# Kernel optimization log

Measured on AMD Instinct MI355X. Metric: run time of the kernel, lower is better.

## Reference

```python
import jax, jax.numpy as jnp
import numpy as np
from jax import lax

STRIDES = (4, 8, 16, 32, 64)
SIZES = (32, 64, 128, 256, 512)
RATIOS = (0.5, 1.0, 2.0)
IMG_H, IMG_W = 1024, 1024
PRE_NMS = 1000
POST_NMS = 1000
NMS_THRESH = 0.7
BBOX_CLIP = float(np.log(1000.0 / 16.0))
NEG_INF = -1e9


def _cell_anchors(size):
    a = []
    for r in RATIOS:
        w = size * np.sqrt(1.0 / r)
        h = size * np.sqrt(r)
        a.append([-w / 2.0, -h / 2.0, w / 2.0, h / 2.0])
    return np.array(a, np.float32)  # [A,4]


def _level_anchors(H, W, stride, size):
    cell = _cell_anchors(size)  # [A,4]
    ys = np.arange(H, dtype=np.float32) * stride
    xs = np.arange(W, dtype=np.float32) * stride
    yy, xx = np.meshgrid(ys, xs, indexing='ij')  # row-major (H,W)
    shifts = np.stack([xx, yy, xx, yy], axis=-1).reshape(-1, 1, 4)
    return jnp.asarray((shifts + cell[None]).reshape(-1, 4))  # [(H*W*A),4] in (H,W,A) order


def conv2d(x, w, b, pad):
    y = lax.conv_general_dilated(x, w, (1, 1), pad,
                                 dimension_numbers=('NCHW', 'OIHW', 'NCHW'))
    return y + b[None, :, None, None]


def decode(deltas, anchors):
    widths = anchors[:, 2] - anchors[:, 0] + 1.0
    heights = anchors[:, 3] - anchors[:, 1] + 1.0
    ctr_x = anchors[:, 0] + 0.5 * widths
    ctr_y = anchors[:, 1] + 0.5 * heights
    dx, dy = deltas[..., 0], deltas[..., 1]
    dw = jnp.minimum(deltas[..., 2], BBOX_CLIP)
    dh = jnp.minimum(deltas[..., 3], BBOX_CLIP)
    pcx = dx * widths + ctr_x
    pcy = dy * heights + ctr_y
    pw = jnp.exp(dw) * widths
    ph = jnp.exp(dh) * heights
    return jnp.stack([pcx - 0.5 * pw, pcy - 0.5 * ph,
                      pcx + 0.5 * pw - 1.0, pcy + 0.5 * ph - 1.0], axis=-1)


def iou_matrix(boxes):
    area = (boxes[:, 2] - boxes[:, 0]) * (boxes[:, 3] - boxes[:, 1])
    lt = jnp.maximum(boxes[:, None, :2], boxes[None, :, :2])
    rb = jnp.minimum(boxes[:, None, 2:], boxes[None, :, 2:])
    wh = jnp.maximum(rb - lt, 0.0)
    inter = wh[..., 0] * wh[..., 1]
    return inter / (area[:, None] + area[None, :] - inter + 1e-9)


def nms_keep(boxes):
    # boxes [N,4] already sorted by score desc; greedy NMS -> bool keep mask
    N = boxes.shape[0]
    iou = iou_matrix(boxes)

    def body(keep, i):
        row = jnp.take(iou, i, axis=0) > NMS_THRESH
        row = row.at[i].set(False)
        keep = jnp.where(keep[i], keep & ~row, keep)
        return keep, None

    keep, _ = lax.scan(body, jnp.ones((N,), bool), jnp.arange(N))
    return keep


def _forward(feats, conv_w, conv_b, cls_w, cls_b, bbox_w, bbox_b):
    level_boxes, level_scores = [], []
    for lvl, feat in enumerate(feats):
        B, _, H, W = feat.shape
        t = jax.nn.relu(conv2d(feat, conv_w, conv_b, 'SAME'))
        logits = conv2d(t, cls_w, cls_b, 'VALID')    # [B,A,H,W]
        breg = conv2d(t, bbox_w, bbox_b, 'VALID')    # [B,4A,H,W]
        A = logits.shape[1]
        scores = jnp.transpose(logits, (0, 2, 3, 1)).reshape(B, -1)            # (H,W,A)
        deltas = breg.reshape(B, A, 4, H, W).transpose(0, 3, 4, 1, 2).reshape(B, -1, 4)
        anchors = _level_anchors(H, W, STRIDES[lvl], SIZES[lvl])
        boxes = decode(deltas, anchors)  # [B,N,4]
        boxes = jnp.stack([jnp.clip(boxes[..., 0], 0.0, IMG_W - 1.0),
                           jnp.clip(boxes[..., 1], 0.0, IMG_H - 1.0),
                           jnp.clip(boxes[..., 2], 0.0, IMG_W - 1.0),
                           jnp.clip(boxes[..., 3], 0.0, IMG_H - 1.0)], axis=-1)
        k = min(PRE_NMS, scores.shape[1])
        top_s, idx = lax.top_k(scores, k)                                   # [B,k]
        top_b = jnp.take_along_axis(boxes, idx[..., None], axis=1)          # [B,k,4]
        keep = jax.vmap(nms_keep)(top_b)                                    # [B,k] bool
        level_scores.append(jnp.where(keep, top_s, NEG_INF))
        level_boxes.append(top_b)
    all_s = jnp.concatenate(level_scores, axis=1)
    all_b = jnp.concatenate(level_boxes, axis=1)
    fs, fi = lax.top_k(all_s, POST_NMS)                                     # [B,POST]
    fb = jnp.take_along_axis(all_b, fi[..., None], axis=1)                  # [B,POST,4]
    return jnp.concatenate([fb, fs[..., None]], axis=-1)                    # [B,POST,5]


def setup_inputs() -> dict:
    key = jax.random.key(0)
    ks = jax.random.split(key, 8)
    C = 256
    feats = {
        'feat0': jax.random.normal(ks[0], (2, C, 256, 256), jnp.float32),
        'feat1': jax.random.normal(ks[1], (2, C, 128, 128), jnp.float32),
        'feat2': jax.random.normal(ks[2], (2, C, 64, 64), jnp.float32),
        'feat3': jax.random.normal(ks[3], (2, C, 32, 32), jnp.float32),
        'feat4': jax.random.normal(ks[4], (2, C, 16, 16), jnp.float32),
    }
    params = {
        'conv_w': jax.random.normal(ks[5], (C, C, 3, 3), jnp.float32) * 0.01,
        'conv_b': jnp.zeros((C,), jnp.float32),
        'cls_w': jax.random.normal(ks[6], (3, C, 1, 1), jnp.float32) * 0.01,
        'cls_b': jnp.zeros((3,), jnp.float32),
        'bbox_w': jax.random.normal(ks[7], (12, C, 1, 1), jnp.float32) * 0.01,
        'bbox_b': jnp.zeros((12,), jnp.float32),
    }
    return {**feats, **params}


def reference(feat0, feat1, feat2, feat3, feat4, conv_w, conv_b, cls_w, cls_b, bbox_w, bbox_b):
    return _forward([feat0, feat1, feat2, feat3, feat4],
                    conv_w, conv_b, cls_w, cls_b, bbox_w, bbox_b)
```

## Files before the change

### kernel.cpp

```cpp
#include <hip/hip_runtime.h>
#include <cmath>


#define NTOT_PER_IMG 261888
#define ATOT_PER_IMG 4768

__constant__ int c_NLVL[5] = {196608, 49152, 12288, 3072, 768};
__constant__ int c_KLVL[5] = {1000, 1000, 1000, 1000, 768};
__constant__ int c_LOFF[5] = {0, 196608, 245760, 258048, 261120};
__constant__ int c_AOFF[5] = {0, 1000, 2000, 3000, 4000};

struct Anch { float cx1[3]; float cy1[3]; };
struct ConvCfg { Anch an[5]; };

__device__ __forceinline__ void ldsWaveFence() {
  asm volatile("s_waitcnt lgkmcnt(0)" ::: "memory");
}

__global__ __launch_bounds__(256) void wtrans(const float* __restrict__ Wsrc,
                                              float* __restrict__ Wt) {
  __shared__ float T[16][17];
  int k0 = blockIdx.x * 16;
  int o0 = blockIdx.y * 16;
  int i = threadIdx.x >> 4, j = threadIdx.x & 15;
  T[i][j] = Wsrc[(size_t)(o0 + i) * 2304 + (k0 + j)];
  __syncthreads();
  Wt[(size_t)(k0 + i) * 256 + (o0 + j)] = T[j][i];
}

__global__ __launch_bounds__(256, 2) void conv_gemm(
    const float* __restrict__ f0, const float* __restrict__ f1,
    const float* __restrict__ f2, const float* __restrict__ f3,
    const float* __restrict__ f4, const float* __restrict__ Wt,
    const float* __restrict__ convb, const float* __restrict__ clsw,
    const float* __restrict__ clsb, const float* __restrict__ bboxw,
    const float* __restrict__ bboxb, float* __restrict__ scoresOut,
    float4* __restrict__ boxesOut, ConvCfg cfg) {
  __shared__ __align__(16) float s_mem[7424];
  __shared__ float s_Red2[272];
  float* const s_tl = s_mem;
  float* const s_xbase = s_mem + 4160;

  int b = blockIdx.x;
  const float* feat;
  int lvl, img, tile, H, logW, stride, lvlOff;
  if (b < 2048) {
    lvl = 0; feat = f0; H = 256; logW = 8; stride = 4; lvlOff = 0;
    img = b >> 10; tile = b & 1023;
  } else if (b < 2560) {
    lvl = 1; feat = f1; H = 128; logW = 7; stride = 8; lvlOff = 196608;
    int r = b - 2048; img = r >> 8; tile = r & 255;
  } else if (b < 2688) {
    lvl = 2; feat = f2; H = 64; logW = 6; stride = 16; lvlOff = 245760;
    int r = b - 2560; img = r >> 6; tile = r & 63;
  } else if (b < 2720) {
    lvl = 3; feat = f3; H = 32; logW = 5; stride = 32; lvlOff = 258048;
    int r = b - 2688; img = r >> 4; tile = r & 15;
  } else {
    lvl = 4; feat = f4; H = 16; logW = 4; stride = 64; lvlOff = 261120;
    int r = b - 2720; img = r >> 2; tile = r & 3;
  }
  const int W = H, HW = H * W;
  const int p0 = tile * 64;
  const float* fimg = feat + (size_t)img * 256 * HW;

  const int log2nc = (logW < 6) ? logW : 6;
  const int ncols = 1 << log2nc;
  const int R = 64 >> log2nc;
  const int py0 = p0 >> logW;
  const int c_start = p0 & (W - 1);
  const int WIN = ncols + 2;
  const int NX = (R + 2) * WIN;

  const int tid = threadIdx.x;
  const int wid = tid >> 6;
  const int lane = tid & 63;
  const int oc0 = (tid >> 3) * 8;
  const int pxg = tid & 7;
  const int px0 = pxg * 8;
  const int trow = px0 >> log2nc;
  const int tcol0 = px0 & (ncols - 1);

  float* const s_xw = s_xbase + wid * 816;

  int goffX[4], loffX[4];
#pragma unroll
  for (int s = 0; s < 4; s++) {
    int idx = lane + 64 * s;
    goffX[s] = -1; loffX[s] = -1;
    if (idx < NX) {
      int lr = idx / WIN;
      int lc = idx - lr * WIN;
      int sy = py0 - 1 + lr;
      int sx = c_start - 1 + lc;
      loffX[s] = lr * 68 + lc;
      if (sy >= 0 && sy < H && sx >= 0 && sx < W) goffX[s] = sy * W + sx;
    }
  }

  float acc[8][8];
#pragma unroll
  for (int i = 0; i < 8; i++)
#pragma unroll
    for (int p = 0; p < 8; p++) acc[i][p] = 0.f;

#pragma unroll
  for (int s = 0; s < 4; s++)
    if (loffX[s] >= 0)
      s_xw[loffX[s]] = (goffX[s] >= 0) ? fimg[goffX[s]] : 0.f;
  ldsWaveFence();

#pragma unroll 1
  for (int ic = 0; ic < 256; ic++) {
    const float* xb = s_xw + (ic & 1) * 408;

    float pxv[4];
    if (ic < 255) {
      const float* fnext = fimg + (size_t)(ic + 1) * HW;
#pragma unroll
      for (int s = 0; s < 4; s++)
        pxv[s] = (goffX[s] >= 0) ? fnext[goffX[s]] : 0.f;
    }

    const float* wic = Wt + (size_t)ic * 2304 + oc0;
#pragma unroll 1
    for (int ky = 0; ky < 3; ky++) {
      const float* xr = xb + (trow + ky) * 68 + tcol0;
      float4 xA = *(const float4*)(xr);
      float4 xB = *(const float4*)(xr + 4);
      float2 xC = *(const float2*)(xr + 8);
      float xw[10] = {xA.x, xA.y, xA.z, xA.w,
                      xB.x, xB.y, xB.z, xB.w, xC.x, xC.y};
      const float* wky = wic + ky * 768;
#pragma unroll
      for (int kx = 0; kx < 3; kx++) {
        float4 wa = *(const float4*)(wky + kx * 256);
        float4 wc = *(const float4*)(wky + kx * 256 + 4);
        float wv[8] = {wa.x, wa.y, wa.z, wa.w, wc.x, wc.y, wc.z, wc.w};
#pragma unroll
        for (int i = 0; i < 8; i++)
#pragma unroll
          for (int p = 0; p < 8; p++)
            acc[i][p] = __builtin_fmaf(wv[i], xw[p + kx], acc[i][p]);
      }
    }

    if (ic < 255) {
      float* xn = s_xw + ((ic + 1) & 1) * 408;
#pragma unroll
      for (int s = 0; s < 4; s++)
        if (loffX[s] >= 0) xn[loffX[s]] = pxv[s];
    }
    ldsWaveFence();
  }

  float cb[8];
#pragma unroll
  for (int i = 0; i < 8; i++) cb[i] = convb[oc0 + i];

  const Anch an = cfg.an[lvl];
  const float BCLIP = (float)4.135166556742356;
  const size_t obase = (size_t)img * NTOT_PER_IMG + lvlOff;

#pragma unroll 1
  for (int r = 0; r < 4; r++) {
    if ((pxg >> 1) == r) {
      int pl = px0 - 16 * r;
#pragma unroll
      for (int p = 0; p < 8; p++) {
        float4 v0 = make_float4(fmaxf(acc[0][p] + cb[0], 0.f),
                                fmaxf(acc[1][p] + cb[1], 0.f),
                                fmaxf(acc[2][p] + cb[2], 0.f),
                                fmaxf(acc[3][p] + cb[3], 0.f));
        float4 v1 = make_float4(fmaxf(acc[4][p] + cb[4], 0.f),
                                fmaxf(acc[5][p] + cb[5], 0.f),
                                fmaxf(acc[6][p] + cb[6], 0.f),
                                fmaxf(acc[7][p] + cb[7], 0.f));
        *(float4*)(s_tl + (pl + p) * 260 + oc0) = v0;
        *(float4*)(s_tl + (pl + p) * 260 + oc0 + 4) = v1;
      }
    }
    __syncthreads();

    if (tid < 240) {
      int px = tid / 15, c = tid - px * 15;
      const float* wr0 = (c < 3) ? (clsw + c * 256) : (bboxw + (c - 3) * 256);
      float bb = (c < 3) ? clsb[c] : bboxb[c - 3];
      const float* trow2 = &s_tl[px * 260];
      float tot = 0.f;
#pragma unroll
      for (int g = 0; g < 16; g++) {
        const float* wr = wr0 + g * 16;
        const float* tr = trow2 + g * 16;
        float s = 0.f;
#pragma unroll
        for (int i = 0; i < 16; i++) s += wr[i] * tr[i];
        tot += s;
      }
      s_Red2[px * 17 + c] = tot + bb;
    }
    __syncthreads();

    if (tid < 48) {
      int px = tid / 3, a = tid - px * 3;
      int pxl = p0 + r * 16 + px;
      int gy = pxl >> logW, gx = pxl & (W - 1);
      float sc = s_Red2[px * 17 + a];
      float dxv = s_Red2[px * 17 + 3 + a * 4 + 0];
      float dyv = s_Red2[px * 17 + 3 + a * 4 + 1];
      float dwv = s_Red2[px * 17 + 3 + a * 4 + 2];
      float dhv = s_Red2[px * 17 + 3 + a * 4 + 3];
      float sx = (float)(gx * stride), sy = (float)(gy * stride);
      float x1 = __fadd_rn(sx, an.cx1[a]);
      float x2 = __fsub_rn(sx, an.cx1[a]);
      float y1 = __fadd_rn(sy, an.cy1[a]);
      float y2 = __fsub_rn(sy, an.cy1[a]);
      float wdt = __fadd_rn(__fsub_rn(x2, x1), 1.0f);
      float hgt = __fadd_rn(__fsub_rn(y2, y1), 1.0f);
      float ctx = __fadd_rn(x1, __fmul_rn(0.5f, wdt));
      float cty = __fadd_rn(y1, __fmul_rn(0.5f, hgt));
      float dw = fminf(dwv, BCLIP), dh = fminf(dhv, BCLIP);
      float pcx = __fadd_rn(__fmul_rn(dxv, wdt), ctx);
      float pcy = __fadd_rn(__fmul_rn(dyv, hgt), cty);
      float pw = __fmul_rn(expf(dw), wdt);
      float ph = __fmul_rn(expf(dh), hgt);
      float hw = __fmul_rn(0.5f, pw), hh = __fmul_rn(0.5f, ph);
      float bx1 = __fsub_rn(pcx, hw);
      float by1 = __fsub_rn(pcy, hh);
      float bx2 = __fsub_rn(__fadd_rn(pcx, hw), 1.0f);
      float by2 = __fsub_rn(__fadd_rn(pcy, hh), 1.0f);
      bx1 = fminf(fmaxf(bx1, 0.f), 1023.f);
      by1 = fminf(fmaxf(by1, 0.f), 1023.f);
      bx2 = fminf(fmaxf(bx2, 0.f), 1023.f);
      by2 = fminf(fmaxf(by2, 0.f), 1023.f);
      size_t o = obase + (size_t)pxl * 3 + a;
      scoresOut[o] = sc;
      boxesOut[o] = make_float4(bx1, by1, bx2, by2);
    }
    __syncthreads();
  }
}

__device__ __forceinline__ unsigned fkey(float f) {
  unsigned b = __float_as_uint(f);
  return (b & 0x80000000u) ? ~b : (b | 0x80000000u);
}
__device__ __forceinline__ float funkey(unsigned u) {
  unsigned b = (u & 0x80000000u) ? (u & 0x7fffffffu) : ~u;
  return __uint_as_float(b);
}

template <bool FINAL>
__global__ __launch_bounds__(1024) void topk_kernel(
    const float* __restrict__ scoresIn, const float4* __restrict__ boxesIn,
    float* __restrict__ scoresOut, float4* __restrict__ boxesOut,
    float* __restrict__ finalOut) {
  __shared__ unsigned long long keys[1024];
  __shared__ unsigned hist[256];
  __shared__ unsigned s_comm[4];
  int lvl = 0, img, N, k;
  const float* src;
  const float4* bsrc;
  if (FINAL) {
    img = blockIdx.x; N = ATOT_PER_IMG; k = 1000;
    src = scoresIn + (size_t)img * ATOT_PER_IMG;
    bsrc = boxesIn + (size_t)img * ATOT_PER_IMG;
  } else {
    lvl = blockIdx.x; img = blockIdx.y;
    N = c_NLVL[lvl]; k = c_KLVL[lvl];
    src = scoresIn + (size_t)img * NTOT_PER_IMG + c_LOFF[lvl];
    bsrc = boxesIn + (size_t)img * NTOT_PER_IMG + c_LOFF[lvl];
  }
  const int tid = threadIdx.x;

  unsigned pref = 0, pmask = 0, krem = (unsigned)k, cntT = 0;
  for (int pass = 3; pass >= 0; pass--) {
    int shift = pass * 8;
    if (tid < 256) hist[tid] = 0;
    __syncthreads();
    for (int i = tid; i < N; i += 1024) {
      unsigned u = fkey(src[i]);
      if ((u & pmask) == pref) atomicAdd(&hist[(u >> shift) & 255], 1u);
    }
    __syncthreads();
    if (tid == 0) {
      unsigned cum = 0;
      for (int d = 255; d >= 0; d--) {
        unsigned c = hist[d];
        if (cum + c >= krem) {
          s_comm[0] = krem - cum; s_comm[1] = c; s_comm[2] = (unsigned)d;
          break;
        }
        cum += c;
      }
    }
    __syncthreads();
    krem = s_comm[0]; cntT = s_comm[1];
    pref |= s_comm[2] << shift;
    pmask |= 0xFFu << shift;
    __syncthreads();
  }
  const unsigned T = pref, r = krem;
  unsigned m = (unsigned)N;
  if (r < cntT) {
    unsigned lo = 0, hi = (unsigned)N;
    while (lo < hi) {
      unsigned mid = (lo + hi) >> 1;
      if (tid == 0) s_comm[3] = 0;
      __syncthreads();
      for (unsigned i = tid; i < mid; i += 1024)
        if (fkey(src[i]) == T) atomicAdd(&s_comm[3], 1u);
      __syncthreads();
      unsigned c = s_comm[3];
      __syncthreads();
      if (c >= r) hi = mid; else lo = mid + 1;
    }
    m = lo;
  }
  if (tid == 0) s_comm[3] = 0;
  __syncthreads();
  for (int i = tid; i < N; i += 1024) {
    unsigned u = fkey(src[i]);
    if (u > T || (u == T && (unsigned)i < m)) {
      unsigned p = atomicAdd(&s_comm[3], 1u);
      if (p < 1024)
        keys[p] = ((unsigned long long)u << 32) | (unsigned)(~(unsigned)i);
    }
  }
  __syncthreads();
  if (tid >= k) keys[tid] = 0ull;
  __syncthreads();
  for (unsigned k2 = 2; k2 <= 1024; k2 <<= 1) {
    for (unsigned j = k2 >> 1; j > 0; j >>= 1) {
      unsigned i = tid, ixj = i ^ j;
      if (ixj > i) {
        unsigned long long a = keys[i], b = keys[ixj];
        bool sw = ((i & k2) == 0) ? (a < b) : (a > b);
        if (sw) { keys[i] = b; keys[ixj] = a; }
      }
      __syncthreads();
    }
  }
  if (tid < k) {
    unsigned long long key = keys[tid];
    unsigned u = (unsigned)(key >> 32);
    unsigned idx = ~((unsigned)key);
    float sc = funkey(u);
    float4 b = bsrc[idx];
    if (FINAL) {
      float* o = finalOut + ((size_t)img * 1000 + tid) * 5;
      o[0] = b.x; o[1] = b.y; o[2] = b.z; o[3] = b.w; o[4] = sc;
    } else {
      scoresOut[(size_t)img * ATOT_PER_IMG + c_AOFF[lvl] + tid] = sc;
      boxesOut[(size_t)img * ATOT_PER_IMG + c_AOFF[lvl] + tid] = b;
    }
  }
}

__global__ __launch_bounds__(256) void nms_matrix(
    const float4* __restrict__ allb, unsigned long long* __restrict__ supp) {
  int lvl = blockIdx.x, img = blockIdx.y, rb = blockIdx.z;
  int k = c_KLVL[lvl];
  int task = img * 5 + lvl;
  const float4* src = allb + (size_t)img * ATOT_PER_IMG + c_AOFF[lvl];
  __shared__ float4 bb[1000];
  __shared__ float ar[1000];
  for (int j = threadIdx.x; j < k; j += 256) {
    float4 b = src[j];
    bb[j] = b;
    ar[j] = __fmul_rn(__fsub_rn(b.z, b.x), __fsub_rn(b.w, b.y));
  }
  __syncthreads();
  int i = rb * 256 + threadIdx.x;
  if (i < k) {
    float4 bi = bb[i];
    float ai = ar[i];
    unsigned long long* row = supp + ((size_t)task * 1024 + i) * 16;
    int jw0 = i >> 6;
    for (int jw = 0; jw < jw0; jw++) row[jw] = 0ull;
    for (int jw = jw0; jw < 16; jw++) {
      unsigned long long bits = 0;
      int jbase = jw * 64;
      for (int jj = 0; jj < 64; jj++) {
        int j = jbase + jj;
        if (j > i && j < k) {
          float4 bj = bb[j];
          float ltx = fmaxf(bi.x, bj.x), lty = fmaxf(bi.y, bj.y);
          float rbx = fminf(bi.z, bj.z), rby = fminf(bi.w, bj.w);
          float wx = fmaxf(__fsub_rn(rbx, ltx), 0.f);
          float wy = fmaxf(__fsub_rn(rby, lty), 0.f);
          float inter = __fmul_rn(wx, wy);
          float den = __fadd_rn(__fsub_rn(__fadd_rn(ai, ar[j]), inter), 1e-9f);
          if (__fdiv_rn(inter, den) > 0.7f) bits |= 1ull << jj;
        }
      }
      row[jw] = bits;
    }
  }
}

__global__ __launch_bounds__(64) void nms_scan(
    const float* __restrict__ topS, const unsigned long long* __restrict__ supp,
    float* __restrict__ fscore) {
  int lvl = blockIdx.x, img = blockIdx.y;
  int k = c_KLVL[lvl];
  int task = img * 5 + lvl;
  int lane = threadIdx.x;
  const unsigned long long* base = supp + (size_t)task * 1024 * 16;
  unsigned long long rem = 0, keep = 0;
  for (int b0 = 0; b0 < k; b0 += 16) {
    unsigned long long buf[16];
#pragma unroll
    for (int t = 0; t < 16; t++) {
      int i = b0 + t;
      buf[t] = (lane < 16 && i < k) ? base[(size_t)i * 16 + lane] : 0ull;
    }
#pragma unroll
    for (int t = 0; t < 16; t++) {
      int i = b0 + t;
      if (i >= k) break;
      int wi = i >> 6, bi = i & 63;
      unsigned long long rw = __shfl(rem, wi);
      if (!((rw >> bi) & 1ull)) {
        rem |= buf[t];
        if (lane == wi) keep |= (1ull << bi);
      }
    }
  }
  const float* ts = topS + (size_t)img * ATOT_PER_IMG + c_AOFF[lvl];
  float* fs = fscore + (size_t)img * ATOT_PER_IMG + c_AOFF[lvl];
  for (int i = lane; i < k; i += 64) {
    int wi = i >> 6;
    unsigned long long kw = __shfl(keep, wi);
    fs[i] = ((kw >> (i & 63)) & 1ull) ? ts[i] : -1e9f;
  }
}

static Anch mkAnch(double size) {
  Anch a;
  const double R[3] = {0.5, 1.0, 2.0};
  for (int i = 0; i < 3; i++) {
    double w = size * sqrt(1.0 / R[i]);
    double h = size * sqrt(R[i]);
    a.cx1[i] = (float)(-w / 2.0);
    a.cy1[i] = (float)(-h / 2.0);
  }
  return a;
}

extern "C" void kernel_launch(void* const* d_in, const int* in_sizes, int n_in,
                              void* d_out, int out_size, void* d_ws,
                              size_t ws_size, hipStream_t stream) {
  (void)in_sizes; (void)n_in; (void)out_size; (void)ws_size;
  const float* f0 = (const float*)d_in[0];
  const float* f1 = (const float*)d_in[1];
  const float* f2 = (const float*)d_in[2];
  const float* f3 = (const float*)d_in[3];
  const float* f4 = (const float*)d_in[4];
  const float* conv_w = (const float*)d_in[5];
  const float* conv_b = (const float*)d_in[6];
  const float* cls_w  = (const float*)d_in[7];
  const float* cls_b  = (const float*)d_in[8];
  const float* bbox_w = (const float*)d_in[9];
  const float* bbox_b = (const float*)d_in[10];
  float* out = (float*)d_out;

  float* wsf = (float*)d_ws;
  float* Wt     = wsf;
  float* scores = Wt + 589824;
  float* boxes  = scores + 2 * NTOT_PER_IMG;
  float* topS   = boxes + (size_t)2 * NTOT_PER_IMG * 4;
  float* allb   = topS + 2 * ATOT_PER_IMG;
  float* fscore = allb + (size_t)2 * ATOT_PER_IMG * 4;
  unsigned long long* supp =
      (unsigned long long*)(fscore + 2 * ATOT_PER_IMG);

  wtrans<<<dim3(144, 16), 256, 0, stream>>>(conv_w, Wt);

  ConvCfg cfg;
  const double SZ[5] = {32, 64, 128, 256, 512};
  for (int l = 0; l < 5; l++) cfg.an[l] = mkAnch(SZ[l]);

  conv_gemm<<<2728, 256, 0, stream>>>(f0, f1, f2, f3, f4, Wt, conv_b, cls_w,
                                      cls_b, bbox_w, bbox_b, scores,
                                      (float4*)boxes, cfg);

  topk_kernel<false><<<dim3(5, 2), 1024, 0, stream>>>(
      scores, (const float4*)boxes, topS, (float4*)allb, nullptr);
  nms_matrix<<<dim3(5, 2, 4), 256, 0, stream>>>((const float4*)allb, supp);
  nms_scan<<<dim3(5, 2), 64, 0, stream>>>(topS, supp, fscore);
  topk_kernel<true><<<2, 1024, 0, stream>>>(
      fscore, (const float4*)allb, nullptr, nullptr, out);
}
```

Before: 3.584 ms.

## Software-pipeline conv weight loads with register double buffering across ky rows

Restructures the 3x3 conv inner loop to process two input channels per iteration. Weight float4 loads for the next ky row are held in two register sets (A/B) and issued one stage ahead of the FMAs, hiding global load latency. The per-channel LDS fence is removed and the input-tile stores are interleaved between stages. This raises register pressure under launch_bounds(256,2) and relies on the wave-private LDS buffers staying ordered without explicit waits.

```diff
diff --git a/kernel.cpp b/kernel.cpp
--- a/kernel.cpp
+++ b/kernel.cpp
@@ -16,6 +16,56 @@
 __device__ __forceinline__ void ldsWaveFence() {
   asm volatile("s_waitcnt lgkmcnt(0)" ::: "memory");
 }
+
+__device__ __forceinline__ void fma_block(
+    float acc[8][8],
+    const float4& w0, const float4& w1, const float4& w2,
+    const float4& w3, const float4& w4, const float4& w5,
+    const float4& xA, const float4& xB, const float2& xC) {
+  float xw[10] = {xA.x, xA.y, xA.z, xA.w,
+                  xB.x, xB.y, xB.z, xB.w, xC.x, xC.y};
+  {
+    float wv[8] = {w0.x, w0.y, w0.z, w0.w, w1.x, w1.y, w1.z, w1.w};
+#pragma unroll
+    for (int i = 0; i < 8; i++)
+#pragma unroll
+      for (int p = 0; p < 8; p++)
+        acc[i][p] = __builtin_fmaf(wv[i], xw[p + 0], acc[i][p]);
+  }
+  {
+    float wv[8] = {w2.x, w2.y, w2.z, w2.w, w3.x, w3.y, w3.z, w3.w};
+#pragma unroll
+    for (int i = 0; i < 8; i++)
+#pragma unroll
+      for (int p = 0; p < 8; p++)
+        acc[i][p] = __builtin_fmaf(wv[i], xw[p + 1], acc[i][p]);
+  }
+  {
+    float wv[8] = {w4.x, w4.y, w4.z, w4.w, w5.x, w5.y, w5.z, w5.w};
+#pragma unroll
+    for (int i = 0; i < 8; i++)
+#pragma unroll
+      for (int p = 0; p < 8; p++)
+        acc[i][p] = __builtin_fmaf(wv[i], xw[p + 2], acc[i][p]);
+  }
+}
+
+#define STAGE(C0, C1, C2, C3, C4, C5, N0, N1, N2, N3, N4, N5, nbase, xrow) \
+  do {                                                                     \
+    asm volatile("" ::: "memory");                                         \
+    const float* nb_ = (nbase);                                            \
+    N0 = *(const float4*)(nb_);                                            \
+    N1 = *(const float4*)(nb_ + 4);                                        \
+    N2 = *(const float4*)(nb_ + 256);                                      \
+    N3 = *(const float4*)(nb_ + 260);                                      \
+    N4 = *(const float4*)(nb_ + 512);                                      \
+    N5 = *(const float4*)(nb_ + 516);                                      \
+    const float* xr_ = (xrow);                                             \
+    float4 xA_ = *(const float4*)(xr_);                                    \
+    float4 xB_ = *(const float4*)(xr_ + 4);                                \
+    float2 xC_ = *(const float2*)(xr_ + 8);                                \
+    fma_block(acc, C0, C1, C2, C3, C4, C5, xA_, xB_, xC_);                 \
+  } while (0)
 
 __global__ __launch_bounds__(256) void wtrans(const float* __restrict__ Wsrc,
                                               float* __restrict__ Wt) {
@@ -81,7 +131,8 @@
   const int trow = px0 >> log2nc;
   const int tcol0 = px0 & (ncols - 1);
 
-  float* const s_xw = s_xbase + wid * 816;
+  float* const buf0 = s_xbase + wid * 816;
+  float* const buf1 = buf0 + 408;
 
   int goffX[4], loffX[4];
 #pragma unroll
@@ -107,51 +158,71 @@
 #pragma unroll
   for (int s = 0; s < 4; s++)
     if (loffX[s] >= 0)
-      s_xw[loffX[s]] = (goffX[s] >= 0) ? fimg[goffX[s]] : 0.f;
+      buf0[loffX[s]] = (goffX[s] >= 0) ? fimg[goffX[s]] : 0.f;
   ldsWaveFence();
 
+  float4 A0, A1, A2, A3, A4, A5, B0, B1, B2, B3, B4, B5;
+  {
+    const float* wb = Wt + oc0;
+    A0 = *(const float4*)(wb);
+    A1 = *(const float4*)(wb + 4);
+    A2 = *(const float4*)(wb + 256);
+    A3 = *(const float4*)(wb + 260);
+    A4 = *(const float4*)(wb + 512);
+    A5 = *(const float4*)(wb + 516);
+  }
+
+  const float* xr0 = buf0 + trow * 68 + tcol0;
+  const float* xr1 = buf1 + trow * 68 + tcol0;
+
 #pragma unroll 1
-  for (int ic = 0; ic < 256; ic++) {
-    const float* xb = s_xw + (ic & 1) * 408;
-
-    float pxv[4];
-    if (ic < 255) {
-      const float* fnext = fimg + (size_t)(ic + 1) * HW;
+  for (int icc = 0; icc < 128; icc++) {
+    const int ic0 = icc * 2, ic1 = ic0 + 1;
+    const int ic2 = (ic0 + 2 < 256) ? ic0 + 2 : 0;
+
+    float pxA[4];
+    {
+      const float* fp = fimg + (size_t)ic1 * HW;
 #pragma unroll
       for (int s = 0; s < 4; s++)
-        pxv[s] = (goffX[s] >= 0) ? fnext[goffX[s]] : 0.f;
-    }
-
-    const float* wic = Wt + (size_t)ic * 2304 + oc0;
-#pragma unroll 1
-    for (int ky = 0; ky < 3; ky++) {
-      const float* xr = xb + (trow + ky) * 68 + tcol0;
-      float4 xA = *(const float4*)(xr);
-      float4 xB = *(const float4*)(xr + 4);
-      float2 xC = *(const float2*)(xr + 8);
-      float xw[10] = {xA.x, xA.y, xA.z, xA.w,
-                      xB.x, xB.y, xB.z, xB.w, xC.x, xC.y};
-      const float* wky = wic + ky * 768;
-#pragma unroll
-      for (int kx = 0; kx < 3; kx++) {
-        float4 wa = *(const float4*)(wky + kx * 256);
-        float4 wc = *(const float4*)(wky + kx * 256 + 4);
-        float wv[8] = {wa.x, wa.y, wa.z, wa.w, wc.x, wc.y, wc.z, wc.w};
-#pragma unroll
-        for (int i = 0; i < 8; i++)
-#pragma unroll
-          for (int p = 0; p < 8; p++)
-            acc[i][p] = __builtin_fmaf(wv[i], xw[p + kx], acc[i][p]);
-      }
-    }
-
-    if (ic < 255) {
-      float* xn = s_xw + ((ic + 1) & 1) * 408;
+        pxA[s] = (goffX[s] >= 0) ? fp[goffX[s]] : 0.f;
+    }
+
+    const float* w_ic0 = Wt + (size_t)ic0 * 2304 + oc0;
+    const float* w_ic1 = w_ic0 + 2304;
+    const float* w_ic2 = Wt + (size_t)ic2 * 2304 + oc0;
+
+    STAGE(A0, A1, A2, A3, A4, A5, B0, B1, B2, B3, B4, B5,
+          w_ic0 + 768, xr0);
+#pragma unroll
+    for (int s = 0; s < 4; s++)
+      if (loffX[s] >= 0) buf1[loffX[s]] = pxA[s];
+
+    STAGE(B0, B1, B2, B3, B4, B5, A0, A1, A2, A3, A4, A5,
+          w_ic0 + 1536, xr0 + 68);
+
+    float pxB[4];
+    {
+      const float* fp = fimg + (size_t)ic2 * HW;
 #pragma unroll
       for (int s = 0; s < 4; s++)
-        if (loffX[s] >= 0) xn[loffX[s]] = pxv[s];
-    }
-    ldsWaveFence();
+        pxB[s] = (goffX[s] >= 0) ? fp[goffX[s]] : 0.f;
+    }
+
+    STAGE(A0, A1, A2, A3, A4, A5, B0, B1, B2, B3, B4, B5,
+          w_ic1, xr0 + 136);
+
+    STAGE(B0, B1, B2, B3, B4, B5, A0, A1, A2, A3, A4, A5,
+          w_ic1 + 768, xr1);
+#pragma unroll
+    for (int s = 0; s < 4; s++)
+      if (loffX[s] >= 0) buf0[loffX[s]] = pxB[s];
+
+    STAGE(A0, A1, A2, A3, A4, A5, B0, B1, B2, B3, B4, B5,
+          w_ic1 + 1536, xr1 + 68);
+
+    STAGE(B0, B1, B2, B3, B4, B5, A0, A1, A2, A3, A4, A5,
+          w_ic2, xr1 + 136);
   }
 
   float cb[8];
```

Result: slower. 3.774 ms (+5.3%).
